# Performance work log

Measured on AMD Instinct MI355X. Metric: run time of the kernel, lower is better.

Reference implementation:

```python
import jax, jax.numpy as jnp
import numpy as np

B, N, T, F_FEAT, T_OUT = 256, 512, 12, 12, 12
HID = 3 * N           # 1536, LSTM hidden size
IN = N * F_FEAT       # 6144, LSTM input size


def setup_inputs() -> dict:
    key = jax.random.key(0)
    ks = jax.random.split(key, 8)
    stdv = 1.0 / np.sqrt(HID)
    u = lambda k, shape, s: jax.random.uniform(k, shape, jnp.float32, -s, s)
    return {
        "A_hat": jax.random.normal(ks[0], (N, N), jnp.float32),
        "X": jax.random.normal(ks[1], (B, N, T, F_FEAT), jnp.float32),
        "W_ih": u(ks[2], (4 * HID, IN), stdv),
        "W_hh": u(ks[3], (4 * HID, HID), stdv),
        "b_ih": u(ks[4], (4 * HID,), stdv),
        "b_hh": u(ks[5], (4 * HID,), stdv),
        "lin_W": u(ks[6], (T_OUT, 3 * T), 1.0 / np.sqrt(3 * T)),
        "lin_b": u(ks[7], (T_OUT,), 1.0 / np.sqrt(3 * T)),
    }


def reference(A_hat, X, W_ih, W_hh, b_ih, b_hh, lin_W, lin_b):
    # (B, N, T, F) -> (B, N*T, F) -> (F, B, N*T); loop axis is the feature dim
    out1 = X.reshape(B, N * T, F_FEAT).transpose(2, 0, 1)

    def step(carry, x_t):  # x_t: (B, N*T)
        h, c = carry
        gates = x_t @ W_ih.T + b_ih + h @ W_hh.T + b_hh  # (B, 4*HID)
        i, f, g, o = jnp.split(gates, 4, axis=-1)        # PyTorch gate order i,f,g,o
        c = jax.nn.sigmoid(f) * c + jax.nn.sigmoid(i) * jnp.tanh(g)
        h = jax.nn.sigmoid(o) * jnp.tanh(c)
        h = jnp.tanh(h)  # extra tanh applied in the original forward
        return (h, c), h

    init = (jnp.zeros((B, HID), X.dtype), jnp.zeros((B, HID), X.dtype))
    _, hs = jax.lax.scan(step, init, out1)          # (F, B, HID)
    al = hs.transpose(1, 2, 0)                      # (B, 3N, F) == torch.cat of unsqueezed states
    out2 = al.reshape(B, N, 3 * T)                  # (B, N, 3T)
    out3 = jax.nn.relu(out2) @ lin_W.T + lin_b      # (B, N, T_OUT)
    return out3
```

## Files before the change

### kernel.cpp

```cpp
#include <hip/hip_runtime.h>
#include <hip/hip_bf16.h>
#include <stdint.h>

typedef uint16_t u16;
typedef __attribute__((ext_vector_type(8))) __bf16 bf16x8;
typedef __attribute__((ext_vector_type(4))) float f32x4;
typedef __attribute__((ext_vector_type(4))) u16 u16x4;

#define BSZ   256
#define NN    512
#define TT    12
#define FF    12
#define HID   1536
#define INSZ  6144
#define GATES 6144
#define MROWS 3072

static __device__ __forceinline__ u16 f2bf(float x) {
  uint32_t u = __builtin_bit_cast(uint32_t, x);
  u += 0x7fffu + ((u >> 16) & 1u);
  return (u16)(u >> 16);
}

static __device__ __forceinline__ float sigm(float x) {
  return 1.0f / (1.0f + expf(-x));
}

__global__ void cvt_perm(const float* __restrict__ in, u16* __restrict__ out,
                         int ncol4) {
  long idx = (long)blockIdx.x * blockDim.x + threadIdx.x;
  int r  = (int)(idx / ncol4);
  int c4 = (int)(idx - (long)r * ncol4);
  int rp = ((r % HID) << 2) + r / HID;
  float4 v = ((const float4*)in)[idx];
  u16x4 w = { f2bf(v.x), f2bf(v.y), f2bf(v.z), f2bf(v.w) };
  ((u16x4*)out)[(size_t)rp * ncol4 + c4] = w;
}

__global__ void pack_x4(const float* __restrict__ X, u16* __restrict__ Ax) {
  int idx = blockIdx.x * blockDim.x + threadIdx.x;
  int b  = idx / (INSZ / 4);
  int k4 = idx - b * (INSZ / 4);
  const float* xp = X + (size_t)b * (INSZ * FF) + (size_t)k4 * (4 * FF);
  float4 v[12];
#pragma unroll
  for (int j = 0; j < 12; ++j) v[j] = ((const float4*)xp)[j];
  const float* vf = (const float*)v;
#pragma unroll
  for (int f = 0; f < FF; ++f) {
    u16x4 w = { f2bf(vf[0 * FF + f]), f2bf(vf[1 * FF + f]),
                f2bf(vf[2 * FF + f]), f2bf(vf[3 * FF + f]) };
    *(u16x4*)&Ax[(size_t)(f * BSZ + b) * INSZ + k4 * 4] = w;
  }
}

#define BM8 192
#define BN8 384
#define LDSA_SZ 24576
#define LDSB_SZ 49152
#define LDS_TOTAL (2 * (LDSA_SZ + LDSB_SZ))

#define GLL(src, dst)                                                          \
  __builtin_amdgcn_global_load_lds(                                            \
      (const __attribute__((address_space(1))) void*)(src),                    \
      (__attribute__((address_space(3))) void*)(dst), 16, 0, 0)

#define SBAR() asm volatile("s_barrier" ::: "memory")
#define SCHED_FENCE_DS() __builtin_amdgcn_sched_barrier(0x7F)
#define WAIT_LGKM0()                                                           \
  do {                                                                         \
    asm volatile("s_waitcnt lgkmcnt(0)" ::: "memory");                         \
    __builtin_amdgcn_sched_barrier(0);                                         \
  } while (0)

__global__ __launch_bounds__(512, 1) void gemm8p(
    const u16* __restrict__ A, const u16* __restrict__ Bt,
    const float* __restrict__ bi, const float* __restrict__ bh,
    float* __restrict__ C, int M, int N, int K) {
  extern __shared__ __align__(16) char lds[];
  const int tid  = threadIdx.x;
  const int lane = tid & 63;
  const int wid  = tid >> 6;
  const int wr   = wid >> 2;
  const int wc   = wid & 3;

  const int nbx  = N / BN8;
  const int cpx  = gridDim.x >> 3;
  const int orig = blockIdx.x;
  const int wgid = (orig & 7) * cpx + (orig >> 3);
  const int m0   = (wgid / nbx) * BM8;
  const int n0   = (wgid % nbx) * BN8;

  const int fr    = lane & 15;
  const int kb    = (lane >> 4) << 4;
  const int swz   = (fr & 7) << 4;
  const int colp0 = kb ^ swz;
  const int colp1 = (64 | kb) ^ swz;

  const int srow = tid >> 3;
  const int scb  = ((tid & 7) << 4) ^ ((srow & 7) << 4);
  const u16* gA = A  + (size_t)(m0 + srow) * K + (scb >> 1);
  const u16* gB = Bt + (size_t)(n0 + srow) * K + (scb >> 1);
  const int wdst = wid << 10;

  char* ldsA = lds;
  char* ldsB = lds + 2 * LDSA_SZ;
  char* aRowB = ldsA + (wr * 96 + fr) * 128;
  char* bRowB = ldsB + (wc * 96 + fr) * 128;

  f32x4 acc[6][6] = {};
  const int NT = K >> 6;

#pragma unroll
  for (int c = 0; c < 3; ++c) GLL(gA + (size_t)c * 64 * K, ldsA + c * 8192 + wdst);
#pragma unroll
  for (int c = 0; c < 6; ++c) GLL(gB + (size_t)c * 64 * K, ldsB + c * 8192 + wdst);

  for (int t = 0; t < NT; ++t) {
    const int p = t & 1;
    char* aRow = aRowB + p * LDSA_SZ;
    char* bRow = bRowB + p * LDSB_SZ;
    char* An = ldsA + (p ^ 1) * LDSA_SZ;
    char* Bn = ldsB + (p ^ 1) * LDSB_SZ;
    const u16* gAn = gA + (size_t)(t + 1) * 64;
    const u16* gBn = gB + (size_t)(t + 1) * 64;
    const bool pf = (t + 1 < NT);

    bf16x8 a0[2][3], a1[2][3], b0[2][3], b1[2][3];

    if (pf) {
#pragma unroll
      for (int c = 0; c < 3; ++c) GLL(gAn + (size_t)c * 64 * K, An + c * 8192 + wdst);
      asm volatile("s_waitcnt vmcnt(3)" ::: "memory");
    } else {
      asm volatile("s_waitcnt vmcnt(0)" ::: "memory");
    }
    SBAR();

#pragma unroll
    for (int i = 0; i < 3; ++i) {
      a0[0][i] = *(const bf16x8*)(aRow + i * 2048 + colp0);
      a0[1][i] = *(const bf16x8*)(aRow + i * 2048 + colp1);
      b0[0][i] = *(const bf16x8*)(bRow + i * 2048 + colp0);
      b0[1][i] = *(const bf16x8*)(bRow + i * 2048 + colp1);
    }
    __builtin_amdgcn_s_setprio(1);
#pragma unroll
    for (int i = 0; i < 3; ++i)
#pragma unroll
      for (int j = 0; j < 3; ++j) {
        acc[i][j] = __builtin_amdgcn_mfma_f32_16x16x32_bf16(a0[0][i], b0[0][j], acc[i][j], 0, 0, 0);
        acc[i][j] = __builtin_amdgcn_mfma_f32_16x16x32_bf16(a0[1][i], b0[1][j], acc[i][j], 0, 0, 0);
      }
    __builtin_amdgcn_s_setprio(0);
    if (pf) {
      GLL(gBn + (size_t)0 * 64 * K, Bn + 0 * 8192 + wdst);
      GLL(gBn + (size_t)1 * 64 * K, Bn + 1 * 8192 + wdst);
    }
    SCHED_FENCE_DS();

#pragma unroll
    for (int i = 0; i < 3; ++i) {
      b1[0][i] = *(const bf16x8*)(bRow + (3 + i) * 2048 + colp0);
      b1[1][i] = *(const bf16x8*)(bRow + (3 + i) * 2048 + colp1);
    }
    __builtin_amdgcn_s_setprio(1);
#pragma unroll
    for (int i = 0; i < 3; ++i)
#pragma unroll
      for (int j = 0; j < 3; ++j) {
        acc[i][3 + j] = __builtin_amdgcn_mfma_f32_16x16x32_bf16(a0[0][i], b1[0][j], acc[i][3 + j], 0, 0, 0);
        acc[i][3 + j] = __builtin_amdgcn_mfma_f32_16x16x32_bf16(a0[1][i], b1[1][j], acc[i][3 + j], 0, 0, 0);
      }
    __builtin_amdgcn_s_setprio(0);
    if (pf) {
      GLL(gBn + (size_t)2 * 64 * K, Bn + 2 * 8192 + wdst);
      GLL(gBn + (size_t)3 * 64 * K, Bn + 3 * 8192 + wdst);
    }
    SCHED_FENCE_DS();

#pragma unroll
    for (int i = 0; i < 3; ++i) {
      a1[0][i] = *(const bf16x8*)(aRow + (3 + i) * 2048 + colp0);
      a1[1][i] = *(const bf16x8*)(aRow + (3 + i) * 2048 + colp1);
    }
    __builtin_amdgcn_s_setprio(1);
#pragma unroll
    for (int i = 0; i < 3; ++i)
#pragma unroll
      for (int j = 0; j < 3; ++j) {
        acc[3 + i][3 + j] = __builtin_amdgcn_mfma_f32_16x16x32_bf16(a1[0][i], b1[0][j], acc[3 + i][3 + j], 0, 0, 0);
        acc[3 + i][3 + j] = __builtin_amdgcn_mfma_f32_16x16x32_bf16(a1[1][i], b1[1][j], acc[3 + i][3 + j], 0, 0, 0);
      }
    __builtin_amdgcn_s_setprio(0);
    if (pf) {
      GLL(gBn + (size_t)4 * 64 * K, Bn + 4 * 8192 + wdst);
      GLL(gBn + (size_t)5 * 64 * K, Bn + 5 * 8192 + wdst);
    }
    SCHED_FENCE_DS();

    __builtin_amdgcn_s_setprio(1);
#pragma unroll
    for (int i = 0; i < 3; ++i)
#pragma unroll
      for (int j = 0; j < 3; ++j) {
        acc[3 + i][j] = __builtin_amdgcn_mfma_f32_16x16x32_bf16(a1[0][i], b0[0][j], acc[3 + i][j], 0, 0, 0);
        acc[3 + i][j] = __builtin_amdgcn_mfma_f32_16x16x32_bf16(a1[1][i], b0[1][j], acc[3 + i][j], 0, 0, 0);
      }
    __builtin_amdgcn_s_setprio(0);

    SBAR();
  }

  const int r0 = (lane >> 4) << 2;
  const int cc = lane & 15;
#pragma unroll
  for (int j = 0; j < 6; ++j) {
    const int col = n0 + wc * 96 + j * 16 + cc;
    const int oc  = (col & 3) * HID + (col >> 2);
    const float bv = bi[oc] + bh[oc];
#pragma unroll
    for (int i = 0; i < 6; ++i) {
      const size_t rbase = (size_t)(m0 + wr * 96 + i * 16 + r0) * N + col;
#pragma unroll
      for (int r = 0; r < 4; ++r)
        C[rbase + (size_t)r * N] = acc[i][j][r] + bv;
    }
  }
}

__global__ __launch_bounds__(256, 4) void gemm_cell(
    const u16* __restrict__ hbf_in,
    const u16* __restrict__ Whhb,
    const float* __restrict__ XW_f,
    float* __restrict__ cbuf,
    u16* __restrict__ hbf_out,
    float* __restrict__ hs_f) {
  __shared__ __align__(16) char lds[32768];
  const int tid  = threadIdx.x;
  const int lane = tid & 63;
  const int wid  = tid >> 6;
  const int wr   = wid >> 1;
  const int wc   = wid & 1;
  const int n0   = blockIdx.x * 64;
  const int m0   = blockIdx.y * 64;
  const int K    = HID;

  const int fr    = lane & 15;
  const int kb    = (lane >> 4) << 4;
  const int swz   = (fr & 7) << 4;
  const int colp0 = kb ^ swz;
  const int colp1 = (64 | kb) ^ swz;

  const int srow = tid >> 3;
  const int scb  = ((tid & 7) << 4) ^ ((srow & 7) << 4);
  const u16* gA = hbf_in + (size_t)(m0 + srow) * K + (scb >> 1);
  const u16* gB = Whhb   + (size_t)(n0 + srow) * K + (scb >> 1);
  const int wdst = wid << 10;

  char* ldsA = lds;
  char* ldsB = lds + 16384;
  char* aRowB = ldsA + (wr * 32 + fr) * 128;
  char* bRowB = ldsB + (wc * 32 + fr) * 128;

  f32x4 acc[2][2] = {};
  const int NT = K >> 6;

  GLL(gA,                  ldsA + wdst);
  GLL(gA + (size_t)32 * K, ldsA + 4096 + wdst);
  GLL(gB,                  ldsB + wdst);
  GLL(gB + (size_t)32 * K, ldsB + 4096 + wdst);

  for (int t = 0; t < NT; ++t) {
    const int p = t & 1;
    char* aRow = aRowB + p * 8192;
    char* bRow = bRowB + p * 8192;
    char* An = ldsA + (p ^ 1) * 8192;
    char* Bn = ldsB + (p ^ 1) * 8192;
    const u16* gAn = gA + (size_t)(t + 1) * 64;
    const u16* gBn = gB + (size_t)(t + 1) * 64;

    if (t + 1 < NT) {
      GLL(gAn,                  An + wdst);
      GLL(gAn + (size_t)32 * K, An + 4096 + wdst);
      GLL(gBn,                  Bn + wdst);
      GLL(gBn + (size_t)32 * K, Bn + 4096 + wdst);
      asm volatile("s_waitcnt vmcnt(4)" ::: "memory");
    } else {
      asm volatile("s_waitcnt vmcnt(0)" ::: "memory");
    }
    SBAR();

    bf16x8 a[2][2], b[2][2];
#pragma unroll
    for (int i = 0; i < 2; ++i) {
      a[0][i] = *(const bf16x8*)(aRow + i * 2048 + colp0);
      a[1][i] = *(const bf16x8*)(aRow + i * 2048 + colp1);
      b[0][i] = *(const bf16x8*)(bRow + i * 2048 + colp0);
      b[1][i] = *(const bf16x8*)(bRow + i * 2048 + colp1);
    }
    WAIT_LGKM0();
    __builtin_amdgcn_s_setprio(1);
#pragma unroll
    for (int i = 0; i < 2; ++i)
#pragma unroll
      for (int j = 0; j < 2; ++j) {
        acc[i][j] = __builtin_amdgcn_mfma_f32_16x16x32_bf16(a[0][i], b[0][j], acc[i][j], 0, 0, 0);
        acc[i][j] = __builtin_amdgcn_mfma_f32_16x16x32_bf16(a[1][i], b[1][j], acc[i][j], 0, 0, 0);
      }
    __builtin_amdgcn_s_setprio(0);
    SBAR();
  }

  float* sacc = (float*)lds;
  const int r0 = (lane >> 4) << 2;
  const int cc = lane & 15;
#pragma unroll
  for (int i = 0; i < 2; ++i)
#pragma unroll
    for (int j = 0; j < 2; ++j) {
      const int ml = wr * 32 + i * 16 + r0;
      const int nl = wc * 32 + j * 16 + cc;
#pragma unroll
      for (int r = 0; r < 4; ++r)
        sacc[(ml + r) * 68 + nl] = acc[i][j][r];
    }
  __syncthreads();

  for (int it = tid; it < 1024; it += 256) {
    const int bl = it >> 4;
    const int jl = it & 15;
    const int b  = m0 + bl;
    const int jg = (n0 >> 2) + jl;
    const float4 hw = *(const float4*)&sacc[bl * 68 + jl * 4];
    const float4 xw = *(const float4*)&XW_f[(size_t)b * GATES + n0 + jl * 4];
    const float gi = xw.x + hw.x;
    const float gf = xw.y + hw.y;
    const float gg = xw.z + hw.z;
    const float go = xw.w + hw.w;
    const int cidx = b * HID + jg;
    const float cp = cbuf[cidx];
    const float cv = sigm(gf) * cp + sigm(gi) * tanhf(gg);
    const float h  = tanhf(sigm(go) * tanhf(cv));
    cbuf[cidx]    = cv;
    hbf_out[cidx] = f2bf(h);
    hs_f[cidx]    = h;
  }
}

__global__ void cell_first(const float* __restrict__ XW,
                           float* __restrict__ cbuf,
                           u16* __restrict__ hbf_out,
                           float* __restrict__ hs_f) {
  int it = blockIdx.x * blockDim.x + threadIdx.x;
  int b = it / HID;
  int j = it - b * HID;
  const float4 xw = *(const float4*)&XW[(size_t)b * GATES + 4 * j];
  const float cv = sigm(xw.x) * tanhf(xw.z);
  const float h  = tanhf(sigm(xw.w) * tanhf(cv));
  cbuf[it]    = cv;
  hbf_out[it] = f2bf(h);
  hs_f[it]    = h;
}

__global__ __launch_bounds__(256) void final_k(const float* __restrict__ hs,
                                               const float* __restrict__ lin_W,
                                               const float* __restrict__ lin_b,
                                               float* __restrict__ out) {
  __shared__ float Wsh[12 * 36];
  __shared__ float bsh[12];
  for (int i = threadIdx.x; i < 12 * 36; i += blockDim.x) Wsh[i] = lin_W[i];
  if (threadIdx.x < 12) bsh[threadIdx.x] = lin_b[threadIdx.x];
  __syncthreads();

  int idx = blockIdx.x * blockDim.x + threadIdx.x;
  int b = idx >> 9;
  int n = idx & 511;

  float acc[12];
#pragma unroll
  for (int o = 0; o < 12; ++o) acc[o] = bsh[o];

#pragma unroll
  for (int kk = 0; kk < 3; ++kk)
#pragma unroll
    for (int f = 0; f < 12; ++f) {
      float v = hs[(size_t)(f * BSZ + b) * HID + 3 * n + kk];
      v = fmaxf(v, 0.0f);
      int j = 12 * kk + f;
#pragma unroll
      for (int o = 0; o < 12; ++o) acc[o] += v * Wsh[o * 36 + j];
    }

#pragma unroll
  for (int o = 0; o < 12; ++o) out[(size_t)idx * 12 + o] = acc[o];
}

extern "C" void kernel_launch(void* const* d_in, const int* in_sizes, int n_in,
                              void* d_out, int out_size, void* d_ws, size_t ws_size,
                              hipStream_t stream) {
  (void)in_sizes; (void)n_in; (void)out_size; (void)ws_size;
  const float* X     = (const float*)d_in[1];
  const float* W_ih  = (const float*)d_in[2];
  const float* W_hh  = (const float*)d_in[3];
  const float* b_ih  = (const float*)d_in[4];
  const float* b_hh  = (const float*)d_in[5];
  const float* lin_W = (const float*)d_in[6];
  const float* lin_b = (const float*)d_in[7];
  float* out = (float*)d_out;

  char* p = (char*)d_ws;
  u16*   Ax   = (u16*)p;   p += (size_t)MROWS * INSZ * 2;
  u16*   Wihb = (u16*)p;   p += (size_t)GATES * INSZ * 2;
  u16*   Whhb = (u16*)p;   p += (size_t)GATES * HID * 2;
  float* XW   = (float*)p; p += (size_t)MROWS * GATES * 4;
  u16*   hbfA = (u16*)p;   p += (size_t)BSZ * HID * 2;
  u16*   hbfB = (u16*)p;   p += (size_t)BSZ * HID * 2;
  float* cbuf = (float*)p; p += (size_t)BSZ * HID * 4;
  float* hs   = (float*)p; p += (size_t)FF * BSZ * HID * 4;

  hipFuncSetAttribute((const void*)gemm8p,
                      hipFuncAttributeMaxDynamicSharedMemorySize, LDS_TOTAL);

  cvt_perm<<<(GATES * (INSZ / 4)) / 256, 256, 0, stream>>>(W_ih, Wihb, INSZ / 4);
  cvt_perm<<<(GATES * (HID / 4)) / 256, 256, 0, stream>>>(W_hh, Whhb, HID / 4);
  pack_x4<<<(BSZ * INSZ / 4) / 256, 256, 0, stream>>>(X, Ax);

  gemm8p<<<256, 512, LDS_TOTAL, stream>>>(Ax, Wihb, b_ih, b_hh, XW,
                                          MROWS, GATES, INSZ);

  u16* bufs[2] = { hbfA, hbfB };
  cell_first<<<(BSZ * HID) / 256, 256, 0, stream>>>(XW, cbuf, bufs[0], hs);
  for (int f = 1; f < FF; ++f) {
    gemm_cell<<<dim3(96, 4), 256, 0, stream>>>(
        bufs[(f - 1) & 1], Whhb, XW + (size_t)f * BSZ * GATES, cbuf,
        bufs[f & 1], hs + (size_t)f * BSZ * HID);
  }

  final_k<<<(BSZ * NN) / 256, 256, 0, stream>>>(hs, lin_W, lin_b, out);
}
```

Baseline: 438.6 us.

## Split big-GEMM MFMA phases by K-half and deepen recurrent GEMM K-tile

The input-projection GEMM inner loop is split into eight 9-MFMA phases, one per K-half and quadrant, so each phase waits on fewer LDS fragment loads and LDS reads interleave more finely with MFMAs. The recurrent h@W_hh GEMM K-tile is doubled from 64 to 128, which halves the number of barrier-separated iterations but doubles LDS use to 64KB and lowers launch bounds occupancy from 4 to 2 blocks. The aim is to cut per-iteration sync and latency overhead, at the cost of occupancy in the recurrent kernel and more register pressure.

```diff
diff --git a/kernel.cpp b/kernel.cpp
--- a/kernel.cpp
+++ b/kernel.cpp
@@ -71,6 +71,16 @@
   do {                                                                         \
     asm volatile("s_waitcnt lgkmcnt(0)" ::: "memory");                         \
     __builtin_amdgcn_sched_barrier(0);                                         \
+  } while (0)
+
+#define MFMA9(AF, BF, RO, CO)                                                  \
+  do {                                                                         \
+    __builtin_amdgcn_s_setprio(1);                                             \
+    _Pragma("unroll") for (int i = 0; i < 3; ++i)                              \
+        _Pragma("unroll") for (int j = 0; j < 3; ++j)                          \
+            acc[RO + i][CO + j] = __builtin_amdgcn_mfma_f32_16x16x32_bf16(     \
+                AF[i], BF[j], acc[RO + i][CO + j], 0, 0, 0);                   \
+    __builtin_amdgcn_s_setprio(0);                                             \
   } while (0)
 
 __global__ __launch_bounds__(512, 1) void gemm8p(
@@ -140,19 +150,11 @@
 #pragma unroll
     for (int i = 0; i < 3; ++i) {
       a0[0][i] = *(const bf16x8*)(aRow + i * 2048 + colp0);
-      a0[1][i] = *(const bf16x8*)(aRow + i * 2048 + colp1);
       b0[0][i] = *(const bf16x8*)(bRow + i * 2048 + colp0);
-      b0[1][i] = *(const bf16x8*)(bRow + i * 2048 + colp1);
-    }
-    __builtin_amdgcn_s_setprio(1);
-#pragma unroll
-    for (int i = 0; i < 3; ++i)
-#pragma unroll
-      for (int j = 0; j < 3; ++j) {
-        acc[i][j] = __builtin_amdgcn_mfma_f32_16x16x32_bf16(a0[0][i], b0[0][j], acc[i][j], 0, 0, 0);
-        acc[i][j] = __builtin_amdgcn_mfma_f32_16x16x32_bf16(a0[1][i], b0[1][j], acc[i][j], 0, 0, 0);
-      }
-    __builtin_amdgcn_s_setprio(0);
+    }
+#pragma unroll
+    for (int i = 0; i < 3; ++i) b1[0][i] = *(const bf16x8*)(bRow + (3 + i) * 2048 + colp0);
+    MFMA9(a0[0], b0[0], 0, 0);
     if (pf) {
       GLL(gBn + (size_t)0 * 64 * K, Bn + 0 * 8192 + wdst);
       GLL(gBn + (size_t)1 * 64 * K, Bn + 1 * 8192 + wdst);
@@ -160,19 +162,8 @@
     SCHED_FENCE_DS();
 
 #pragma unroll
-    for (int i = 0; i < 3; ++i) {
-      b1[0][i] = *(const bf16x8*)(bRow + (3 + i) * 2048 + colp0);
-      b1[1][i] = *(const bf16x8*)(bRow + (3 + i) * 2048 + colp1);
-    }
-    __builtin_amdgcn_s_setprio(1);
-#pragma unroll
-    for (int i = 0; i < 3; ++i)
-#pragma unroll
-      for (int j = 0; j < 3; ++j) {
-        acc[i][3 + j] = __builtin_amdgcn_mfma_f32_16x16x32_bf16(a0[0][i], b1[0][j], acc[i][3 + j], 0, 0, 0);
-        acc[i][3 + j] = __builtin_amdgcn_mfma_f32_16x16x32_bf16(a0[1][i], b1[1][j], acc[i][3 + j], 0, 0, 0);
-      }
-    __builtin_amdgcn_s_setprio(0);
+    for (int i = 0; i < 3; ++i) a1[0][i] = *(const bf16x8*)(aRow + (3 + i) * 2048 + colp0);
+    MFMA9(a0[0], b1[0], 0, 3);
     if (pf) {
       GLL(gBn + (size_t)2 * 64 * K, Bn + 2 * 8192 + wdst);
       GLL(gBn + (size_t)3 * 64 * K, Bn + 3 * 8192 + wdst);
@@ -180,34 +171,31 @@
     SCHED_FENCE_DS();
 
 #pragma unroll
-    for (int i = 0; i < 3; ++i) {
-      a1[0][i] = *(const bf16x8*)(aRow + (3 + i) * 2048 + colp0);
-      a1[1][i] = *(const bf16x8*)(aRow + (3 + i) * 2048 + colp1);
-    }
-    __builtin_amdgcn_s_setprio(1);
-#pragma unroll
-    for (int i = 0; i < 3; ++i)
-#pragma unroll
-      for (int j = 0; j < 3; ++j) {
-        acc[3 + i][3 + j] = __builtin_amdgcn_mfma_f32_16x16x32_bf16(a1[0][i], b1[0][j], acc[3 + i][3 + j], 0, 0, 0);
-        acc[3 + i][3 + j] = __builtin_amdgcn_mfma_f32_16x16x32_bf16(a1[1][i], b1[1][j], acc[3 + i][3 + j], 0, 0, 0);
-      }
-    __builtin_amdgcn_s_setprio(0);
+    for (int i = 0; i < 3; ++i) a0[1][i] = *(const bf16x8*)(aRow + i * 2048 + colp1);
+    MFMA9(a1[0], b1[0], 3, 3);
     if (pf) {
       GLL(gBn + (size_t)4 * 64 * K, Bn + 4 * 8192 + wdst);
       GLL(gBn + (size_t)5 * 64 * K, Bn + 5 * 8192 + wdst);
     }
     SCHED_FENCE_DS();
 
-    __builtin_amdgcn_s_setprio(1);
-#pragma unroll
-    for (int i = 0; i < 3; ++i)
-#pragma unroll
-      for (int j = 0; j < 3; ++j) {
-        acc[3 + i][j] = __builtin_amdgcn_mfma_f32_16x16x32_bf16(a1[0][i], b0[0][j], acc[3 + i][j], 0, 0, 0);
-        acc[3 + i][j] = __builtin_amdgcn_mfma_f32_16x16x32_bf16(a1[1][i], b0[1][j], acc[3 + i][j], 0, 0, 0);
-      }
-    __builtin_amdgcn_s_setprio(0);
+#pragma unroll
+    for (int i = 0; i < 3; ++i) b0[1][i] = *(const bf16x8*)(bRow + i * 2048 + colp1);
+    MFMA9(a1[0], b0[0], 3, 0);
+    SCHED_FENCE_DS();
+
+#pragma unroll
+    for (int i = 0; i < 3; ++i) b1[1][i] = *(const bf16x8*)(bRow + (3 + i) * 2048 + colp1);
+    MFMA9(a0[1], b0[1], 0, 0);
+    SCHED_FENCE_DS();
+
+#pragma unroll
+    for (int i = 0; i < 3; ++i) a1[1][i] = *(const bf16x8*)(aRow + (3 + i) * 2048 + colp1);
+    MFMA9(a0[1], b1[1], 0, 3);
+    SCHED_FENCE_DS();
+
+    MFMA9(a1[1], b1[1], 3, 3);
+    MFMA9(a1[1], b0[1], 3, 0);
 
     SBAR();
   }
@@ -229,14 +217,14 @@
   }
 }
 
-__global__ __launch_bounds__(256, 4) void gemm_cell(
+__global__ __launch_bounds__(256, 2) void gemm_cell(
     const u16* __restrict__ hbf_in,
     const u16* __restrict__ Whhb,
     const float* __restrict__ XW_f,
     float* __restrict__ cbuf,
     u16* __restrict__ hbf_out,
     float* __restrict__ hs_f) {
-  __shared__ __align__(16) char lds[32768];
+  __shared__ __align__(16) char lds[65536];
   const int tid  = threadIdx.x;
   const int lane = tid & 63;
   const int wid  = tid >> 6;
@@ -246,68 +234,71 @@
   const int m0   = blockIdx.y * 64;
   const int K    = HID;
 
-  const int fr    = lane & 15;
-  const int kb    = (lane >> 4) << 4;
-  const int swz   = (fr & 7) << 4;
-  const int colp0 = kb ^ swz;
-  const int colp1 = (64 | kb) ^ swz;
-
-  const int srow = tid >> 3;
-  const int scb  = ((tid & 7) << 4) ^ ((srow & 7) << 4);
+  const int fr  = lane & 15;
+  const int kb  = (lane >> 4) << 4;
+  const int swz = (fr & 7) << 4;
+  int colp[4];
+#pragma unroll
+  for (int k = 0; k < 4; ++k) colp[k] = (k * 64 + kb) ^ swz;
+
+  const int srow = tid >> 4;
+  const int scb  = ((tid & 15) << 4) ^ ((srow & 7) << 4);
   const u16* gA = hbf_in + (size_t)(m0 + srow) * K + (scb >> 1);
   const u16* gB = Whhb   + (size_t)(n0 + srow) * K + (scb >> 1);
   const int wdst = wid << 10;
 
   char* ldsA = lds;
-  char* ldsB = lds + 16384;
-  char* aRowB = ldsA + (wr * 32 + fr) * 128;
-  char* bRowB = ldsB + (wc * 32 + fr) * 128;
+  char* ldsB = lds + 32768;
+  char* aRowB = ldsA + (wr * 32 + fr) * 256;
+  char* bRowB = ldsB + (wc * 32 + fr) * 256;
 
   f32x4 acc[2][2] = {};
-  const int NT = K >> 6;
-
-  GLL(gA,                  ldsA + wdst);
-  GLL(gA + (size_t)32 * K, ldsA + 4096 + wdst);
-  GLL(gB,                  ldsB + wdst);
-  GLL(gB + (size_t)32 * K, ldsB + 4096 + wdst);
+  const int NT = K >> 7;
+
+#pragma unroll
+  for (int c = 0; c < 4; ++c) {
+    GLL(gA + (size_t)c * 16 * K, ldsA + c * 4096 + wdst);
+    GLL(gB + (size_t)c * 16 * K, ldsB + c * 4096 + wdst);
+  }
 
   for (int t = 0; t < NT; ++t) {
     const int p = t & 1;
-    char* aRow = aRowB + p * 8192;
-    char* bRow = bRowB + p * 8192;
-    char* An = ldsA + (p ^ 1) * 8192;
-    char* Bn = ldsB + (p ^ 1) * 8192;
-    const u16* gAn = gA + (size_t)(t + 1) * 64;
-    const u16* gBn = gB + (size_t)(t + 1) * 64;
+    char* aRow = aRowB + p * 16384;
+    char* bRow = bRowB + p * 16384;
+    char* An = ldsA + (p ^ 1) * 16384;
+    char* Bn = ldsB + (p ^ 1) * 16384;
+    const u16* gAn = gA + (size_t)(t + 1) * 128;
+    const u16* gBn = gB + (size_t)(t + 1) * 128;
 
     if (t + 1 < NT) {
-      GLL(gAn,                  An + wdst);
-      GLL(gAn + (size_t)32 * K, An + 4096 + wdst);
-      GLL(gBn,                  Bn + wdst);
-      GLL(gBn + (size_t)32 * K, Bn + 4096 + wdst);
-      asm volatile("s_waitcnt vmcnt(4)" ::: "memory");
+#pragma unroll
+      for (int c = 0; c < 4; ++c) {
+        GLL(gAn + (size_t)c * 16 * K, An + c * 4096 + wdst);
+        GLL(gBn + (size_t)c * 16 * K, Bn + c * 4096 + wdst);
+      }
+      asm volatile("s_waitcnt vmcnt(8)" ::: "memory");
     } else {
       asm volatile("s_waitcnt vmcnt(0)" ::: "memory");
     }
     SBAR();
 
-    bf16x8 a[2][2], b[2][2];
-#pragma unroll
-    for (int i = 0; i < 2; ++i) {
-      a[0][i] = *(const bf16x8*)(aRow + i * 2048 + colp0);
-      a[1][i] = *(const bf16x8*)(aRow + i * 2048 + colp1);
-      b[0][i] = *(const bf16x8*)(bRow + i * 2048 + colp0);
-      b[1][i] = *(const bf16x8*)(bRow + i * 2048 + colp1);
-    }
+    bf16x8 a[4][2], b[4][2];
+#pragma unroll
+    for (int k = 0; k < 4; ++k)
+#pragma unroll
+      for (int i = 0; i < 2; ++i) {
+        a[k][i] = *(const bf16x8*)(aRow + i * 4096 + colp[k]);
+        b[k][i] = *(const bf16x8*)(bRow + i * 4096 + colp[k]);
+      }
     WAIT_LGKM0();
     __builtin_amdgcn_s_setprio(1);
 #pragma unroll
-    for (int i = 0; i < 2; ++i)
-#pragma unroll
-      for (int j = 0; j < 2; ++j) {
-        acc[i][j] = __builtin_amdgcn_mfma_f32_16x16x32_bf16(a[0][i], b[0][j], acc[i][j], 0, 0, 0);
-        acc[i][j] = __builtin_amdgcn_mfma_f32_16x16x32_bf16(a[1][i], b[1][j], acc[i][j], 0, 0, 0);
-      }
+    for (int k = 0; k < 4; ++k)
+#pragma unroll
+      for (int i = 0; i < 2; ++i)
+#pragma unroll
+        for (int j = 0; j < 2; ++j)
+          acc[i][j] = __builtin_amdgcn_mfma_f32_16x16x32_bf16(a[k][i], b[k][j], acc[i][j], 0, 0, 0);
     __builtin_amdgcn_s_setprio(0);
     SBAR();
   }
```

Result: no change. 431.3 us (-1.7%).
